# Kernel tuning notes

Hardware: AMD Instinct MI355X
Metric: run time of the kernel (lower is better)

Reference implementation:

```python
import jax, jax.numpy as jnp
import numpy as np

NUM_HEADS = 32
NUM_KV_HEADS = 8
HEAD_DIM = 128
HIDDEN = 4096
ROPE_THETA = 10000.0
SLIDING_WINDOW = 1024
NEG_INF = -1e9


def _make_sliding_window_mask(q_len, kv_len, window):
    # additive mask: 0 where attendable (causal AND within window), -inf otherwise
    i = jnp.arange(q_len)[:, None]
    j = jnp.arange(kv_len)[None, :]
    allowed = (j <= i) & (j > i - window)
    return jnp.where(allowed, 0.0, NEG_INF).astype(jnp.float32)[None, None]  # [1,1,q,kv]


def _rope_tables(seq_len, head_dim, theta):
    inv_freq = 1.0 / (theta ** (jnp.arange(0, head_dim, 2, dtype=jnp.float32) / head_dim))
    t = jnp.arange(seq_len, dtype=jnp.float32)
    freqs = jnp.einsum('i,j->ij', t, inv_freq)        # [S, D/2]
    emb = jnp.concatenate([freqs, freqs], axis=-1)     # [S, D]
    return jnp.cos(emb), jnp.sin(emb)


def _rotate_half(x):
    d = x.shape[-1] // 2
    return jnp.concatenate([-x[..., d:], x[..., :d]], axis=-1)


def setup_inputs() -> dict:
    key = jax.random.key(0)
    ks = jax.random.split(key, 5)
    B, S = 1, 2048
    sc = 0.02
    hidden_states = jax.random.normal(ks[0], (B, S, HIDDEN), dtype=jnp.float32)
    Wq = jax.random.normal(ks[1], (HIDDEN, NUM_HEADS * HEAD_DIM), dtype=jnp.float32) * sc
    Wk = jax.random.normal(ks[2], (HIDDEN, NUM_KV_HEADS * HEAD_DIM), dtype=jnp.float32) * sc
    Wv = jax.random.normal(ks[3], (HIDDEN, NUM_KV_HEADS * HEAD_DIM), dtype=jnp.float32) * sc
    Wo = jax.random.normal(ks[4], (NUM_HEADS * HEAD_DIM, HIDDEN), dtype=jnp.float32) * sc
    attention_mask = _make_sliding_window_mask(S, S, SLIDING_WINDOW)
    position_ids = jnp.arange(S, dtype=jnp.int64)[None, :]
    return {"hidden_states": hidden_states, "attention_mask": attention_mask,
            "position_ids": position_ids, "Wq": Wq, "Wk": Wk, "Wv": Wv, "Wo": Wo}


def reference(hidden_states, attention_mask, position_ids, Wq, Wk, Wv, Wo):
    B, S, _ = hidden_states.shape
    # projections
    q = (hidden_states @ Wq).reshape(B, S, NUM_HEADS, HEAD_DIM).transpose(0, 2, 1, 3)      # [B,H,S,D]
    k = (hidden_states @ Wk).reshape(B, S, NUM_KV_HEADS, HEAD_DIM).transpose(0, 2, 1, 3)   # [B,Hk,S,D]
    v = (hidden_states @ Wv).reshape(B, S, NUM_KV_HEADS, HEAD_DIM).transpose(0, 2, 1, 3)
    # RoPE
    cos_t, sin_t = _rope_tables(S, HEAD_DIM, ROPE_THETA)
    cos = cos_t[position_ids][:, None]  # [B,1,S,D]
    sin = sin_t[position_ids][:, None]
    q = q * cos + _rotate_half(q) * sin
    k = k * cos + _rotate_half(k) * sin
    # repeat_kv (GQA): [B,Hk,S,D] -> [B,H,S,D]
    n_rep = NUM_HEADS // NUM_KV_HEADS
    k = jnp.repeat(k, n_rep, axis=1)
    v = jnp.repeat(v, n_rep, axis=1)
    # attention
    scores = jnp.einsum('bhqd,bhkd->bhqk', q, k) / np.sqrt(HEAD_DIM)
    scores = scores + attention_mask
    probs = jax.nn.softmax(scores, axis=-1)
    out = jnp.einsum('bhqk,bhkd->bhqd', probs, v)
    out = out.transpose(0, 2, 1, 3).reshape(B, S, HIDDEN)
    return out @ Wo
```

## Files before the change

kernel.cpp:

```cpp
#include <hip/hip_runtime.h>

typedef __attribute__((ext_vector_type(8))) short short8;
typedef __attribute__((ext_vector_type(4))) short s16x4;
typedef __attribute__((ext_vector_type(4))) float f32x4;
typedef unsigned short u16;
typedef unsigned int u32;

__device__ __forceinline__ u16 f2bf(float f) {
  union { float f; unsigned int u; } v; v.f = f;
  unsigned int r = (v.u + 0x7FFFu + ((v.u >> 16) & 1u)) >> 16;
  return (u16)r;
}
__device__ __forceinline__ float bf2f(u16 b) {
  union { unsigned int u; float f; } v; v.u = ((unsigned int)b) << 16;
  return v.f;
}
__device__ __forceinline__ void load_lds16(const void* g, void* l) {
  __builtin_amdgcn_global_load_lds((const __attribute__((address_space(1))) void*)g,
                                   (__attribute__((address_space(3))) void*)l, 16, 0, 0);
}

__global__ void cvt_f32_bf16_kernel(const float* __restrict__ in, u16* __restrict__ out, int n4) {
  int i = blockIdx.x * blockDim.x + threadIdx.x;
  if (i >= n4) return;
  float4 v = ((const float4*)in)[i];
  ushort4 o;
  o.x = f2bf(v.x); o.y = f2bf(v.y); o.z = f2bf(v.z); o.w = f2bf(v.w);
  ((ushort4*)out)[i] = o;
}

__device__ __forceinline__ void tconv64_tile(const float* __restrict__ W, u16* __restrict__ Wt,
                                             int K, int N, int nb, int kb, int tid) {
  __shared__ float tile[64][65];
  int tx = tid & 15, ty = tid >> 4;
  const float* src = W + (size_t)(kb + ty) * N + nb + tx * 4;
#pragma unroll
  for (int i = 0; i < 4; ++i) {
    float4 v = *(const float4*)(src + (size_t)i * 16 * N);
    tile[ty + i * 16][tx * 4 + 0] = v.x;
    tile[ty + i * 16][tx * 4 + 1] = v.y;
    tile[ty + i * 16][tx * 4 + 2] = v.z;
    tile[ty + i * 16][tx * 4 + 3] = v.w;
  }
  __syncthreads();
  u16* dst = Wt + (size_t)(nb + ty) * K + kb + tx * 4;
#pragma unroll
  for (int i = 0; i < 4; ++i) {
    s16x4 o;
#pragma unroll
    for (int j = 0; j < 4; ++j) o[j] = (short)f2bf(tile[tx * 4 + j][ty + i * 16]);
    *(s16x4*)(dst + (size_t)i * 16 * K) = o;
  }
}

__global__ void tconv3_kernel(const float* __restrict__ Wq, const float* __restrict__ Wk,
                              const float* __restrict__ Wv, u16* __restrict__ WqT,
                              u16* __restrict__ WkvT) {
  int id = blockIdx.x;
  if (id < 4096)      tconv64_tile(Wq, WqT, 4096, 4096, (id & 63) * 64, (id >> 6) * 64, threadIdx.x);
  else if (id < 5120) { int t = id - 4096; tconv64_tile(Wk, WkvT, 4096, 1024, (t & 15) * 64, (t >> 4) * 64, threadIdx.x); }
  else                { int t = id - 5120; tconv64_tile(Wv, WkvT + (size_t)1024 * 4096, 4096, 1024, (t & 15) * 64, (t >> 4) * 64, threadIdx.x); }
}

__global__ void tconv1_kernel(const float* __restrict__ W, u16* __restrict__ Wt) {
  int id = blockIdx.x;
  tconv64_tile(W, Wt, 4096, 4096, (id & 63) * 64, (id >> 6) * 64, threadIdx.x);
}

__global__ void rope_kernel(u16* __restrict__ Qb, u16* __restrict__ Kb) {
  int idx = blockIdx.x * blockDim.x + threadIdx.x;
  u16* X; int ld, hmask, hshift, id; float scale;
  if (idx < 4194304) { X = Qb; ld = 4096; hmask = 31; hshift = 5; id = idx;           scale = 0.12751781828987514f; }
  else               { X = Kb; ld = 1024; hmask = 7;  hshift = 3; id = idx - 4194304; scale = 1.0f; }
  int j = id & 63;
  int t = id >> 6;
  int hh = t & hmask;
  int s = t >> hshift;
  float invf = exp2f(-(float)j * (13.287712379549449f / 64.0f));
  float ang = (float)s * invf;
  float sn, cs;
  sincosf(ang, &sn, &cs);
  u16* p = X + (size_t)s * ld + hh * 128 + j;
  float a = bf2f(p[0]), b = bf2f(p[64]);
  p[0]  = f2bf((a * cs - b * sn) * scale);
  p[64] = f2bf((b * cs + a * sn) * scale);
}

__global__ __launch_bounds__(256, 2) void gemm_kv_kernel(
    const u16* __restrict__ A, const u16* __restrict__ B,
    u16* __restrict__ Kb, u16* __restrict__ Vt, int N, int K) {
  __shared__ u16 As[2][128 * 64];
  __shared__ u16 Bs[2][128 * 64];
  int tid = threadIdx.x, lane = tid & 63, w = tid >> 6;
  int wr = w >> 1, wc = w & 1;
  int g = lane >> 4, q = lane & 15;
  int nbx = gridDim.x;
  int flat = blockIdx.y * nbx + blockIdx.x;
  int cpx = (nbx * gridDim.y) >> 3;
  flat = (flat & 7) * cpx + (flat >> 3);
  int m0 = (flat / nbx) * 128, n0 = (flat % nbx) * 128;
  f32x4 acc[4][4];
#pragma unroll
  for (int i = 0; i < 4; ++i)
#pragma unroll
    for (int j = 0; j < 4; ++j) acc[i][j] = (f32x4){0.f, 0.f, 0.f, 0.f};
  int srow = tid >> 3;
  int scol = ((tid & 7) ^ (srow & 7)) << 3;
  const u16* ga = A + (size_t)(m0 + srow) * K + scol;
  const u16* gb = B + (size_t)(n0 + srow) * K + scol;
  int xorm = (q & 7) << 3;
  int arow = wr * 64 + q;
  int brow = wc * 64 + q;
  int nt = K >> 6;

  auto stage = [&](int buf, int t) {
    const u16* pa = ga + t * 64;
    const u16* pb = gb + t * 64;
#pragma unroll
    for (int it = 0; it < 4; ++it) {
      load_lds16(pa + (size_t)it * 32 * K, (char*)(&As[buf][0]) + (it * 256 + w * 64) * 16);
      load_lds16(pb + (size_t)it * 32 * K, (char*)(&Bs[buf][0]) + (it * 256 + w * 64) * 16);
    }
  };

  stage(0, 0);
  stage(1, 1);
  asm volatile("s_waitcnt vmcnt(8)" ::: "memory");
  __builtin_amdgcn_s_barrier();
  for (int t = 0; t < nt; ++t) {
    int cur = t & 1;
    short8 af[2][4], bfr[2][4];
#pragma unroll
    for (int kb = 0; kb < 2; ++kb) {
      int col = (kb * 32 + g * 8) ^ xorm;
#pragma unroll
      for (int m = 0; m < 4; ++m) af[kb][m]  = *(const short8*)&As[cur][(arow + m * 16) * 64 + col];
#pragma unroll
      for (int n = 0; n < 4; ++n) bfr[kb][n] = *(const short8*)&Bs[cur][(brow + n * 16) * 64 + col];
    }
    asm volatile("s_waitcnt lgkmcnt(0)" ::: "memory");
    __builtin_amdgcn_s_barrier();
    if (t + 2 < nt) stage(cur, t + 2);
    __builtin_amdgcn_sched_barrier(0);
    __builtin_amdgcn_s_setprio(1);
#pragma unroll
    for (int kb = 0; kb < 2; ++kb)
#pragma unroll
      for (int m = 0; m < 4; ++m)
#pragma unroll
        for (int n = 0; n < 4; ++n)
          acc[m][n] = __builtin_amdgcn_mfma_f32_16x16x32_bf16(af[kb][m], bfr[kb][n], acc[m][n], 0, 0, 0);
    __builtin_amdgcn_s_setprio(0);
    if (t + 2 < nt)      { asm volatile("s_waitcnt vmcnt(8)" ::: "memory"); }
    else if (t + 1 < nt) { asm volatile("s_waitcnt vmcnt(0)" ::: "memory"); }
    __builtin_amdgcn_s_barrier();
  }
  int crow = m0 + wr * 64 + g * 4;
  int ccol = n0 + wc * 64 + q;
  if (n0 < 1024) {
#pragma unroll
    for (int m = 0; m < 4; ++m)
#pragma unroll
      for (int n = 0; n < 4; ++n)
#pragma unroll
        for (int r = 0; r < 4; ++r)
          Kb[(size_t)(crow + m * 16 + r) * 1024 + ccol + n * 16] = f2bf(acc[m][n][r]);
  } else {
#pragma unroll
    for (int n = 0; n < 4; ++n) {
      int vcol = ccol + n * 16 - 1024;
#pragma unroll
      for (int m = 0; m < 4; ++m) {
        s16x4 o;
#pragma unroll
        for (int r = 0; r < 4; ++r) o[r] = (short)f2bf(acc[m][n][r]);
        *(s16x4*)(Vt + (size_t)vcol * 2048 + crow + m * 16) = o;
      }
    }
  }
}

template<int OUTF32>
__global__ __launch_bounds__(512, 2) void gemm_wide_kernel(
    const u16* __restrict__ A, const u16* __restrict__ B,
    void* __restrict__ C, int N, int K) {
  __shared__ u16 As[2][128 * 64];
  __shared__ u16 Bs[2][256 * 64];
  int tid = threadIdx.x, lane = tid & 63, wid = tid >> 6;
  int wr = wid >> 2, wc = wid & 3;
  int g = lane >> 4, q = lane & 15;
  int nbx = gridDim.x;
  int id = blockIdx.y * nbx + blockIdx.x;
  int cpx = (nbx * gridDim.y) >> 3;
  int swz = (id & 7) * cpx + (id >> 3);
  int m0 = (swz / nbx) * 128, n0 = (swz % nbx) * 256;
  f32x4 acc[4][4];
#pragma unroll
  for (int i = 0; i < 4; ++i)
#pragma unroll
    for (int j = 0; j < 4; ++j) acc[i][j] = (f32x4){0.f, 0.f, 0.f, 0.f};
  int srow = tid >> 3;
  int scol = ((tid & 7) ^ (srow & 7)) << 3;
  const u16* ga = A + (size_t)(m0 + srow) * K + scol;
  const u16* gb = B + (size_t)(n0 + srow) * K + scol;
  int xorm = (q & 7) << 3;
  int nt = K >> 6;

  auto stage = [&](int buf, int t) {
    const u16* pa = ga + t * 64;
    const u16* pb = gb + t * 64;
#pragma unroll
    for (int it = 0; it < 2; ++it)
      load_lds16(pa + (size_t)it * 64 * K, (char*)(&As[buf][0]) + it * 8192 + tid * 16);
#pragma unroll
    for (int it = 0; it < 4; ++it)
      load_lds16(pb + (size_t)it * 64 * K, (char*)(&Bs[buf][0]) + it * 8192 + tid * 16);
  };

  stage(0, 0);
  stage(1, 1);
  asm volatile("s_waitcnt vmcnt(6)" ::: "memory");
  __builtin_amdgcn_s_barrier();
  for (int t = 0; t < nt; ++t) {
    int cur = t & 1;
    short8 av[2][4], bv[2][4];
#pragma unroll
    for (int kb = 0; kb < 2; ++kb) {
      int col = (kb * 32 + g * 8) ^ xorm;
#pragma unroll
      for (int fm = 0; fm < 4; ++fm)
        av[kb][fm] = *(const short8*)&As[cur][(wr * 64 + fm * 16 + q) * 64 + col];
#pragma unroll
      for (int fn = 0; fn < 4; ++fn)
        bv[kb][fn] = *(const short8*)&Bs[cur][(wc * 64 + fn * 16 + q) * 64 + col];
    }
    asm volatile("s_waitcnt lgkmcnt(0)" ::: "memory");
    __builtin_amdgcn_s_barrier();
    if (t + 2 < nt) stage(cur, t + 2);
    __builtin_amdgcn_sched_barrier(0);
    __builtin_amdgcn_s_setprio(1);
#pragma unroll
    for (int kb = 0; kb < 2; ++kb)
#pragma unroll
      for (int fm = 0; fm < 4; ++fm)
#pragma unroll
        for (int fn = 0; fn < 4; ++fn)
          acc[fm][fn] = __builtin_amdgcn_mfma_f32_16x16x32_bf16(av[kb][fm], bv[kb][fn], acc[fm][fn], 0, 0, 0);
    __builtin_amdgcn_s_setprio(0);
    if (t + 2 < nt)      { asm volatile("s_waitcnt vmcnt(6)" ::: "memory"); }
    else if (t + 1 < nt) { asm volatile("s_waitcnt vmcnt(0)" ::: "memory"); }
    __builtin_amdgcn_s_barrier();
  }
  int crow = m0 + wr * 64 + g * 4;
  int ccol = n0 + wc * 64 + q;
#pragma unroll
  for (int fm = 0; fm < 4; ++fm)
#pragma unroll
    for (int fn = 0; fn < 4; ++fn)
#pragma unroll
      for (int r = 0; r < 4; ++r) {
        size_t off = (size_t)(crow + fm * 16 + r) * N + ccol + fn * 16;
        if (OUTF32) ((float*)C)[off] = acc[fm][fn][r];
        else        ((u16*)C)[off]   = f2bf(acc[fm][fn][r]);
      }
}

__global__ __launch_bounds__(512, 4) void attn_kernel(
    const u16* __restrict__ Q, const u16* __restrict__ Kg,
    const u16* __restrict__ Vt, u16* __restrict__ O) {
  __shared__ u16 Ks[2][64 * 128];
  __shared__ u16 Vs[2][128 * 64];
  int tid = threadIdx.x, lane = tid & 63, w = tid >> 6;
  int wg = w >> 2;
  int g = lane >> 4, q = lane & 15;
  int q0 = blockIdx.x * 128;
  int h = blockIdx.y, hk = h >> 2;
  int qbase = q0 + wg * 64;
  int qrow = qbase + (w & 3) * 16;
  int xorm = (lane & 7) << 3;
  short8 qf[4];
  {
    const u16* qp = Q + (size_t)(qrow + q) * 4096 + h * 128 + g * 8;
#pragma unroll
    for (int kk = 0; kk < 4; ++kk) qf[kk] = *(const short8*)(qp + kk * 32);
  }
  float mrow = -1e30f, lsum = 0.f;
  f32x4 of[8];
#pragma unroll
  for (int d = 0; d < 8; ++d) of[d] = (f32x4){0.f, 0.f, 0.f, 0.f};
  int bjt_lo = (q0 >= 1024) ? ((q0 - 1023) >> 6) : 0;
  int bjt_hi = (q0 + 64) >> 6;
  int wjt_lo = (qbase >= 1024) ? ((qbase - 1023) >> 6) : 0;
  int wjt_hi = qbase >> 6;
  int krow = tid >> 4;
  int kchunk = (tid & 15) ^ (krow & 7);
  const u16* kbase = Kg + (size_t)krow * 1024 + hk * 128 + (kchunk << 3);
  int vrow = tid >> 3;
  int vchunk = (tid & 7) ^ (vrow & 7);
  const u16* vbase = Vt + (size_t)(hk * 128 + vrow) * 2048 + (vchunk << 3);

  auto stageK = [&](int buf, int j0) {
    const u16* gp = kbase + (size_t)j0 * 1024;
#pragma unroll
    for (int it = 0; it < 2; ++it)
      load_lds16(gp + (size_t)it * 32 * 1024, (char*)(&Ks[buf][0]) + it * 8192 + tid * 16);
  };
  auto stageV = [&](int buf, int j0) {
    const u16* gp = vbase + j0;
#pragma unroll
    for (int it = 0; it < 2; ++it)
      load_lds16(gp + (size_t)it * 64 * 2048, (char*)(&Vs[buf][0]) + it * 8192 + tid * 16);
  };

  int cur = 0;
  stageK(0, bjt_lo << 6);
  stageV(0, bjt_lo << 6);
  asm volatile("s_waitcnt vmcnt(0)" ::: "memory");
  __syncthreads();
  for (int jt = bjt_lo; jt <= bjt_hi; ++jt) {
    int j0 = jt << 6;
    if (jt < bjt_hi) { stageK(cur ^ 1, j0 + 64); stageV(cur ^ 1, j0 + 64); }
    if (jt >= wjt_lo && jt <= wjt_hi) {
      f32x4 sf[4];
#pragma unroll
      for (int nt = 0; nt < 4; ++nt) sf[nt] = (f32x4){0.f, 0.f, 0.f, 0.f};
      const u16* ks = &Ks[cur][0];
      __builtin_amdgcn_s_setprio(1);
#pragma unroll
      for (int kk = 0; kk < 4; ++kk) {
        short8 qv = qf[kk];
        int col = (kk * 32 + g * 8) ^ xorm;
#pragma unroll
        for (int nt = 0; nt < 4; ++nt) {
          short8 kf = *(const short8*)&ks[(nt * 16 + q) * 128 + col];
          sf[nt] = __builtin_amdgcn_mfma_f32_16x16x32_bf16(kf, qv, sf[nt], 0, 0, 0);
        }
      }
      __builtin_amdgcn_s_setprio(0);
      float p[4][4];
#pragma unroll
      for (int nt = 0; nt < 4; ++nt)
#pragma unroll
        for (int r = 0; r < 4; ++r) p[nt][r] = sf[nt][r];
      if (j0 + 63 > qrow || j0 + 1009 <= qrow) {
        int qq = qrow + q;
        int kb = j0 + g * 4;
#pragma unroll
        for (int nt = 0; nt < 4; ++nt)
#pragma unroll
          for (int r = 0; r < 4; ++r) {
            int key = kb + nt * 16 + r;
            if (key > qq || key + 1024 <= qq) p[nt][r] = -1e9f;
          }
      }
      float tm = p[0][0];
#pragma unroll
      for (int nt = 0; nt < 4; ++nt)
#pragma unroll
        for (int r = 0; r < 4; ++r) tm = fmaxf(tm, p[nt][r]);
      tm = fmaxf(tm, __shfl_xor(tm, 16));
      tm = fmaxf(tm, __shfl_xor(tm, 32));
      if (__any(tm > mrow + 8.f)) {
        float nm = fmaxf(mrow, tm);
        float sc = __builtin_amdgcn_exp2f(mrow - nm);
        mrow = nm;
        lsum *= sc;
#pragma unroll
        for (int d = 0; d < 8; ++d) of[d] *= sc;
      }
      float ps = 0.f;
#pragma unroll
      for (int nt = 0; nt < 4; ++nt)
#pragma unroll
        for (int r = 0; r < 4; ++r) {
          float e = __builtin_amdgcn_exp2f(p[nt][r] - mrow);
          p[nt][r] = e;
          ps += e;
        }
      ps += __shfl_xor(ps, 16);
      ps += __shfl_xor(ps, 32);
      lsum += ps;
      u32 pk[4][2];
#pragma unroll
      for (int nt = 0; nt < 4; ++nt) {
        pk[nt][0] = __builtin_amdgcn_perm(__float_as_uint(p[nt][1]), __float_as_uint(p[nt][0]), 0x07060302u);
        pk[nt][1] = __builtin_amdgcn_perm(__float_as_uint(p[nt][3]), __float_as_uint(p[nt][2]), 0x07060302u);
      }
      int s0 = q + ((g & 1) ? 32 : 0);
      int s1 = s0 + 16;
      bool hi_sel = g >= 2;
      const u16* vs = &Vs[cur][0];
      __builtin_amdgcn_s_setprio(1);
#pragma unroll
      for (int kh = 0; kh < 2; ++kh) {
        int lo = kh * 2, hi = lo + 1;
        u32 a0 = (u32)__shfl((int)pk[lo][0], s0);
        u32 a1 = (u32)__shfl((int)pk[lo][1], s0);
        u32 b0 = (u32)__shfl((int)pk[hi][0], s0);
        u32 b1 = (u32)__shfl((int)pk[hi][1], s0);
        u32 a2 = (u32)__shfl((int)pk[lo][0], s1);
        u32 a3 = (u32)__shfl((int)pk[lo][1], s1);
        u32 b2 = (u32)__shfl((int)pk[hi][0], s1);
        u32 b3 = (u32)__shfl((int)pk[hi][1], s1);
        union { u32 u[4]; short8 s; } pb;
        pb.u[0] = hi_sel ? b0 : a0;
        pb.u[1] = hi_sel ? b1 : a1;
        pb.u[2] = hi_sel ? b2 : a2;
        pb.u[3] = hi_sel ? b3 : a3;
        int col = (kh * 32 + g * 8) ^ xorm;
#pragma unroll
        for (int dt = 0; dt < 8; ++dt) {
          short8 vv = *(const short8*)&vs[(dt * 16 + q) * 64 + col];
          of[dt] = __builtin_amdgcn_mfma_f32_16x16x32_bf16(vv, pb.s, of[dt], 0, 0, 0);
        }
      }
      __builtin_amdgcn_s_setprio(0);
    }
    asm volatile("s_waitcnt vmcnt(0)" ::: "memory");
    __builtin_amdgcn_s_barrier();
    cur ^= 1;
  }
  float inv = 1.f / lsum;
  u16* op = O + (size_t)(qrow + q) * 4096 + h * 128 + g * 4;
#pragma unroll
  for (int dt = 0; dt < 8; ++dt) {
    s16x4 o4;
#pragma unroll
    for (int r = 0; r < 4; ++r) o4[r] = (short)f2bf(of[dt][r] * inv);
    *(s16x4*)(op + dt * 16) = o4;
  }
}

extern "C" void kernel_launch(void* const* d_in, const int* in_sizes, int n_in,
                              void* d_out, int out_size, void* d_ws, size_t ws_size,
                              hipStream_t stream) {
  (void)in_sizes; (void)n_in; (void)out_size;
  const float* hs = (const float*)d_in[0];
  const float* Wq = (const float*)d_in[3];
  const float* Wk = (const float*)d_in[4];
  const float* Wv = (const float*)d_in[5];
  const float* Wo = (const float*)d_in[6];
  float* out = (float*)d_out;
  char* ws = (char*)d_ws;

  u16* Xb   = (u16*)(ws + 0);
  u16* Wt   = (u16*)(ws + 16777216);
  u16* WkvT = (u16*)(ws + 50331648);
  u16* Qb   = (u16*)(ws + 67108864);
  u16* Kb   = (u16*)(ws + 83886080);
  u16* Vtb  = (u16*)(ws + 88080384);
  u16* Ab   = (u16*)(ws + 96468992);
  if (ws_size < 113246208u) return;

  cvt_f32_bf16_kernel<<<dim3(2097152 / 256), 256, 0, stream>>>(hs, Xb, 2097152);

  tconv3_kernel<<<dim3(6144), 256, 0, stream>>>(Wq, Wk, Wv, Wt, WkvT);

  gemm_wide_kernel<0><<<dim3(16, 16), 512, 0, stream>>>(Xb, Wt, Qb, 4096, 4096);

  gemm_kv_kernel<<<dim3(16, 16), 256, 0, stream>>>(Xb, WkvT, Kb, Vtb, 2048, 4096);

  rope_kernel<<<dim3(20480), 256, 0, stream>>>(Qb, Kb);

  attn_kernel<<<dim3(16, 32), 512, 0, stream>>>(Qb, Kb, Vtb, Ab);

  tconv1_kernel<<<dim3(4096), 256, 0, stream>>>(Wo, Wt);
  gemm_wide_kernel<1><<<dim3(16, 16), 512, 0, stream>>>(Ab, Wt, out, 4096, 4096);
}
```

Before: 325.9 us.

## Use 256x256 GEMM tiles with split-K and separate combine kernels

Replaces the 128x256 wide GEMM with a 256x256-tile GEMM (8x4 accumulator fragments per wave, one block per CU). K is split in two across grid z so the grid stays at 256 blocks. Each half writes to its own buffer and a new elementwise kernel adds the partials. Larger tiles raise arithmetic intensity per LDS load. The cost is extra launches and partial-buffer traffic, an intermediate bf16 rounding of the Q partials before they are summed, and lower occupancy.

```diff
diff --git a/kernel.cpp b/kernel.cpp
--- a/kernel.cpp
+++ b/kernel.cpp
@@ -27,6 +27,25 @@
   ushort4 o;
   o.x = f2bf(v.x); o.y = f2bf(v.y); o.z = f2bf(v.z); o.w = f2bf(v.w);
   ((ushort4*)out)[i] = o;
+}
+
+__global__ void combine_bf16_kernel(u16* __restrict__ d, const u16* __restrict__ p, int n8) {
+  int i = blockIdx.x * blockDim.x + threadIdx.x;
+  if (i >= n8) return;
+  short8 a = ((const short8*)d)[i];
+  short8 b = ((const short8*)p)[i];
+  short8 o;
+#pragma unroll
+  for (int j = 0; j < 8; ++j) o[j] = (short)f2bf(bf2f((u16)a[j]) + bf2f((u16)b[j]));
+  ((short8*)d)[i] = o;
+}
+__global__ void combine_f32_kernel(float* __restrict__ d, const float* __restrict__ p, int n4) {
+  int i = blockIdx.x * blockDim.x + threadIdx.x;
+  if (i >= n4) return;
+  float4 a = ((const float4*)d)[i];
+  float4 b = ((const float4*)p)[i];
+  a.x += b.x; a.y += b.y; a.z += b.z; a.w += b.w;
+  ((float4*)d)[i] = a;
 }
 
 __device__ __forceinline__ void tconv64_tile(const float* __restrict__ W, u16* __restrict__ Wt,
@@ -181,87 +200,130 @@
 }
 
 template<int OUTF32>
-__global__ __launch_bounds__(512, 2) void gemm_wide_kernel(
+__global__ __launch_bounds__(512, 1) void gemm256_kernel(
     const u16* __restrict__ A, const u16* __restrict__ B,
-    void* __restrict__ C, int N, int K) {
-  __shared__ u16 As[2][128 * 64];
+    void* __restrict__ C0, void* __restrict__ C1, int N, int K, int KH) {
+  __shared__ u16 As[2][256 * 64];
   __shared__ u16 Bs[2][256 * 64];
   int tid = threadIdx.x, lane = tid & 63, wid = tid >> 6;
   int wr = wid >> 2, wc = wid & 3;
   int g = lane >> 4, q = lane & 15;
-  int nbx = gridDim.x;
-  int id = blockIdx.y * nbx + blockIdx.x;
-  int cpx = (nbx * gridDim.y) >> 3;
-  int swz = (id & 7) * cpx + (id >> 3);
-  int m0 = (swz / nbx) * 128, n0 = (swz % nbx) * 256;
-  f32x4 acc[4][4];
-#pragma unroll
-  for (int i = 0; i < 4; ++i)
+  int id = blockIdx.z * gridDim.x * gridDim.y + blockIdx.y * gridDim.x + blockIdx.x;
+  int tot = gridDim.x * gridDim.y * gridDim.z;
+  int swz = (id & 7) * (tot >> 3) + (id >> 3);
+  int perh = gridDim.x * gridDim.y;
+  int z = swz / perh, rem = swz % perh;
+  int m0 = (rem / gridDim.x) * 256, n0 = (rem % gridDim.x) * 256;
+  int k0 = z * KH;
+  f32x4 acc[8][4];
+#pragma unroll
+  for (int i = 0; i < 8; ++i)
 #pragma unroll
     for (int j = 0; j < 4; ++j) acc[i][j] = (f32x4){0.f, 0.f, 0.f, 0.f};
   int srow = tid >> 3;
   int scol = ((tid & 7) ^ (srow & 7)) << 3;
-  const u16* ga = A + (size_t)(m0 + srow) * K + scol;
-  const u16* gb = B + (size_t)(n0 + srow) * K + scol;
+  const u16* ga = A + (size_t)(m0 + srow) * K + k0 + scol;
+  const u16* gb = B + (size_t)(n0 + srow) * K + k0 + scol;
   int xorm = (q & 7) << 3;
-  int nt = K >> 6;
+  int arow = wr * 128 + q;
+  int brow = wc * 64 + q;
+  int nt = KH >> 6;
 
   auto stage = [&](int buf, int t) {
     const u16* pa = ga + t * 64;
     const u16* pb = gb + t * 64;
 #pragma unroll
-    for (int it = 0; it < 2; ++it)
+    for (int it = 0; it < 4; ++it) {
       load_lds16(pa + (size_t)it * 64 * K, (char*)(&As[buf][0]) + it * 8192 + tid * 16);
-#pragma unroll
-    for (int it = 0; it < 4; ++it)
       load_lds16(pb + (size_t)it * 64 * K, (char*)(&Bs[buf][0]) + it * 8192 + tid * 16);
+    }
   };
 
   stage(0, 0);
   stage(1, 1);
-  asm volatile("s_waitcnt vmcnt(6)" ::: "memory");
+  asm volatile("s_waitcnt vmcnt(8)" ::: "memory");
   __builtin_amdgcn_s_barrier();
   for (int t = 0; t < nt; ++t) {
     int cur = t & 1;
-    short8 av[2][4], bv[2][4];
-#pragma unroll
-    for (int kb = 0; kb < 2; ++kb) {
-      int col = (kb * 32 + g * 8) ^ xorm;
-#pragma unroll
-      for (int fm = 0; fm < 4; ++fm)
-        av[kb][fm] = *(const short8*)&As[cur][(wr * 64 + fm * 16 + q) * 64 + col];
-#pragma unroll
-      for (int fn = 0; fn < 4; ++fn)
-        bv[kb][fn] = *(const short8*)&Bs[cur][(wc * 64 + fn * 16 + q) * 64 + col];
-    }
+    int col0 = (g * 8) ^ xorm;
+    int col1 = (32 + g * 8) ^ xorm;
+    short8 af[4], bk[4];
+#pragma unroll
+    for (int m = 0; m < 4; ++m) af[m] = *(const short8*)&As[cur][(arow + m * 16) * 64 + col0];
+#pragma unroll
+    for (int n = 0; n < 4; ++n) bk[n] = *(const short8*)&Bs[cur][(brow + n * 16) * 64 + col0];
+    __builtin_amdgcn_s_barrier();
     asm volatile("s_waitcnt lgkmcnt(0)" ::: "memory");
-    __builtin_amdgcn_s_barrier();
-    if (t + 2 < nt) stage(cur, t + 2);
     __builtin_amdgcn_sched_barrier(0);
     __builtin_amdgcn_s_setprio(1);
 #pragma unroll
-    for (int kb = 0; kb < 2; ++kb)
-#pragma unroll
-      for (int fm = 0; fm < 4; ++fm)
-#pragma unroll
-        for (int fn = 0; fn < 4; ++fn)
-          acc[fm][fn] = __builtin_amdgcn_mfma_f32_16x16x32_bf16(av[kb][fm], bv[kb][fn], acc[fm][fn], 0, 0, 0);
+    for (int m = 0; m < 4; ++m)
+#pragma unroll
+      for (int n = 0; n < 4; ++n)
+        acc[m][n] = __builtin_amdgcn_mfma_f32_16x16x32_bf16(af[m], bk[n], acc[m][n], 0, 0, 0);
     __builtin_amdgcn_s_setprio(0);
-    if (t + 2 < nt)      { asm volatile("s_waitcnt vmcnt(6)" ::: "memory"); }
-    else if (t + 1 < nt) { asm volatile("s_waitcnt vmcnt(0)" ::: "memory"); }
-    __builtin_amdgcn_s_barrier();
-  }
-  int crow = m0 + wr * 64 + g * 4;
+    __builtin_amdgcn_s_barrier();
+#pragma unroll
+    for (int m = 0; m < 4; ++m) af[m] = *(const short8*)&As[cur][(arow + (m + 4) * 16) * 64 + col0];
+    __builtin_amdgcn_s_barrier();
+    asm volatile("s_waitcnt lgkmcnt(0)" ::: "memory");
+    __builtin_amdgcn_sched_barrier(0);
+    __builtin_amdgcn_s_setprio(1);
+#pragma unroll
+    for (int m = 0; m < 4; ++m)
+#pragma unroll
+      for (int n = 0; n < 4; ++n)
+        acc[m + 4][n] = __builtin_amdgcn_mfma_f32_16x16x32_bf16(af[m], bk[n], acc[m + 4][n], 0, 0, 0);
+    __builtin_amdgcn_s_setprio(0);
+    __builtin_amdgcn_s_barrier();
+#pragma unroll
+    for (int m = 0; m < 4; ++m) af[m] = *(const short8*)&As[cur][(arow + m * 16) * 64 + col1];
+#pragma unroll
+    for (int n = 0; n < 4; ++n) bk[n] = *(const short8*)&Bs[cur][(brow + n * 16) * 64 + col1];
+    __builtin_amdgcn_s_barrier();
+    asm volatile("s_waitcnt lgkmcnt(0)" ::: "memory");
+    __builtin_amdgcn_sched_barrier(0);
+    __builtin_amdgcn_s_setprio(1);
+#pragma unroll
+    for (int m = 0; m < 4; ++m)
+#pragma unroll
+      for (int n = 0; n < 4; ++n)
+        acc[m][n] = __builtin_amdgcn_mfma_f32_16x16x32_bf16(af[m], bk[n], acc[m][n], 0, 0, 0);
+    __builtin_amdgcn_s_setprio(0);
+    __builtin_amdgcn_s_barrier();
+#pragma unroll
+    for (int m = 0; m < 4; ++m) af[m] = *(const short8*)&As[cur][(arow + (m + 4) * 16) * 64 + col1];
+    __builtin_amdgcn_s_barrier();
+    asm volatile("s_waitcnt lgkmcnt(0)" ::: "memory");
+    __builtin_amdgcn_sched_barrier(0);
+    __builtin_amdgcn_s_setprio(1);
+#pragma unroll
+    for (int m = 0; m < 4; ++m)
+#pragma unroll
+      for (int n = 0; n < 4; ++n)
+        acc[m + 4][n] = __builtin_amdgcn_mfma_f32_16x16x32_bf16(af[m], bk[n], acc[m + 4][n], 0, 0, 0);
+    __builtin_amdgcn_s_setprio(0);
+    __builtin_amdgcn_s_barrier();
+    if (t + 2 < nt) {
+      stage(cur, t + 2);
+      asm volatile("s_waitcnt vmcnt(8)" ::: "memory");
+    } else if (t + 1 < nt) {
+      asm volatile("s_waitcnt vmcnt(0)" ::: "memory");
+    }
+    __builtin_amdgcn_s_barrier();
+  }
+  int crow = m0 + wr * 128 + g * 4;
   int ccol = n0 + wc * 64 + q;
-#pragma unroll
-  for (int fm = 0; fm < 4; ++fm)
+  void* dst = z ? C1 : C0;
+#pragma unroll
+  for (int fm = 0; fm < 8; ++fm)
 #pragma unroll
     for (int fn = 0; fn < 4; ++fn)
 #pragma unroll
       for (int r = 0; r < 4; ++r) {
         size_t off = (size_t)(crow + fm * 16 + r) * N + ccol + fn * 16;
-        if (OUTF32) ((float*)C)[off] = acc[fm][fn][r];
-        else        ((u16*)C)[off]   = f2bf(acc[fm][fn][r]);
+        if (OUTF32) ((float*)dst)[off] = acc[fm][fn][r];
+        else        ((u16*)dst)[off]   = f2bf(acc[fm][fn][r]);
       }
 }
 
@@ -450,13 +512,16 @@
   u16* Kb   = (u16*)(ws + 83886080);
   u16* Vtb  = (u16*)(ws + 88080384);
   u16* Ab   = (u16*)(ws + 96468992);
+  u16* P1q  = Ab;
+  float* P1o = (float*)(ws + 50331648);
   if (ws_size < 113246208u) return;
 
   cvt_f32_bf16_kernel<<<dim3(2097152 / 256), 256, 0, stream>>>(hs, Xb, 2097152);
 
   tconv3_kernel<<<dim3(6144), 256, 0, stream>>>(Wq, Wk, Wv, Wt, WkvT);
 
-  gemm_wide_kernel<0><<<dim3(16, 16), 512, 0, stream>>>(Xb, Wt, Qb, 4096, 4096);
+  gemm256_kernel<0><<<dim3(16, 8, 2), 512, 0, stream>>>(Xb, Wt, Qb, P1q, 4096, 4096, 2048);
+  combine_bf16_kernel<<<dim3(4096), 256, 0, stream>>>(Qb, P1q, 1048576);
 
   gemm_kv_kernel<<<dim3(16, 16), 256, 0, stream>>>(Xb, WkvT, Kb, Vtb, 2048, 4096);
 
@@ -465,5 +530,6 @@
   attn_kernel<<<dim3(16, 32), 512, 0, stream>>>(Qb, Kb, Vtb, Ab);
 
   tconv1_kernel<<<dim3(4096), 256, 0, stream>>>(Wo, Wt);
-  gemm_wide_kernel<1><<<dim3(16, 16), 512, 0, stream>>>(Ab, Wt, out, 4096, 4096);
-}
+  gemm256_kernel<1><<<dim3(16, 8, 2), 512, 0, stream>>>(Ab, Wt, out, P1o, 4096, 4096, 2048);
+  combine_f32_kernel<<<dim3(8192), 256, 0, stream>>>(out, P1o, 2097152);
+}
```

After: 358.0 us. 1.1x slower.
